# Optimization experiments

Hardware: AMD Instinct MI355X
Metric: run time of the kernel (lower is better)

The kernel has to match this reference:

```python
import jax, jax.numpy as jnp
import numpy as np

ROPE_BASE = 10000.0

def apply_rope(x):
    # x: [B, S, H, Dh]  (rotate-half / NeoX convention)
    B, S, H, Dh = x.shape
    inv_freq = 1.0 / (ROPE_BASE ** (jnp.arange(0, Dh, 2, dtype=jnp.float32) / Dh))  # [Dh/2]
    ang = jnp.arange(S, dtype=jnp.float32)[:, None] * inv_freq[None, :]             # [S, Dh/2]
    cos = jnp.cos(ang)[None, :, None, :].astype(x.dtype)  # [1,S,1,Dh/2]
    sin = jnp.sin(ang)[None, :, None, :].astype(x.dtype)
    x1, x2 = jnp.split(x, 2, axis=-1)
    return jnp.concatenate([x1 * cos - x2 * sin, x1 * sin + x2 * cos], axis=-1)

def setup_inputs() -> dict:
    key = jax.random.key(0)
    k1, k2, k3 = jax.random.split(key, 3)
    B, S, D = 2, 2048, 1024
    x = jax.random.normal(k1, (B, S, D), dtype=jnp.float32)
    attn_mask = jnp.ones((B, S), dtype=bool)
    qkv_w = jax.random.normal(k2, (D, 3 * D), dtype=jnp.float32) * (1.0 / np.sqrt(D))
    out_w = jax.random.normal(k3, (D, D), dtype=jnp.float32) * (1.0 / np.sqrt(D))
    return {"x": x, "qkv_w": qkv_w, "out_w": out_w, "attn_mask": attn_mask, "is_causal": 1}

def reference(x, qkv_w, out_w, attn_mask, is_causal):
    B, S, D = x.shape
    H = 16
    Dh = D // H
    qkv = x @ qkv_w                                  # [B,S,3D]
    q, k, v = jnp.split(qkv, 3, axis=-1)
    q = apply_rope(q.reshape(B, S, H, Dh))           # [B,S,H,Dh]
    k = apply_rope(k.reshape(B, S, H, Dh))
    v = v.reshape(B, S, H, Dh)
    scale = 1.0 / np.sqrt(Dh)
    att = jnp.einsum('bqhd,bkhd->bhqk', q, k) * scale  # [B,H,S,S]
    if is_causal:
        mask = jnp.tril(jnp.ones((S, S), dtype=bool))[None, None]
    else:
        mask = attn_mask[:, None, None, :]             # [B,1,1,S]
    att = jnp.where(mask, att, jnp.finfo(att.dtype).min)
    p = jax.nn.softmax(att, axis=-1)
    y = jnp.einsum('bhqk,bkhd->bqhd', p, v).reshape(B, S, D)
    return y @ out_w
```

## Files before the change

### kernel.cpp

```cpp
#include <hip/hip_runtime.h>
#include <hip/hip_bf16.h>

#define BB 2
#define SS 2048
#define DD 1024
#define HH 16
#define N3 3072

typedef __attribute__((ext_vector_type(8))) short bf16x8;
typedef __attribute__((ext_vector_type(4))) float f32x4;
typedef __attribute__((ext_vector_type(2))) unsigned int u32x2;

__device__ __forceinline__ float b2f(unsigned short u) {
    return __uint_as_float(((unsigned int)u) << 16);
}
__device__ __forceinline__ unsigned short f2b(float f) {
    unsigned int x = __float_as_uint(f);
    x += 0x7fffu + ((x >> 16) & 1u);
    return (unsigned short)(x >> 16);
}
__device__ __forceinline__ unsigned int pack2bf(float a, float b) {
    __hip_bfloat162 h = __float22bfloat162_rn(make_float2(a, b));
    return *(unsigned int*)&h;
}
__device__ __forceinline__ void storeC(float* p, float v) { *p = v; }
__device__ __forceinline__ void storeC(unsigned short* p, float v) { *p = f2b(v); }

__device__ __forceinline__ void gload_lds16(const void* g, void* l) {
    __builtin_amdgcn_global_load_lds(
        (__attribute__((address_space(1))) void*)g,
        (__attribute__((address_space(3))) void*)l, 16, 0, 0);
}

__global__ __launch_bounds__(256) void sincos_tab(float2* __restrict__ tab) {
    int i = blockIdx.x * 256 + threadIdx.x;
    int t = i & 31;
    int s = i >> 5;
    float inv = powf(10000.0f, -(float)t * (1.0f / 32.0f));
    float sn, c;
    sincosf((float)s * inv, &sn, &c);
    tab[i] = make_float2(c, sn);
}

__global__ __launch_bounds__(256) void cast_f32_bf16(
    const float* __restrict__ src, unsigned short* __restrict__ dst)
{
    int i = (blockIdx.x * 256 + threadIdx.x) * 4;
    float4 f = *(const float4*)(src + i);
    uint2 o;
    o.x = pack2bf(f.x, f.y);
    o.y = pack2bf(f.z, f.w);
    *(uint2*)(dst + i) = o;
}

__global__ __launch_bounds__(256) void cast_transpose(
    const float* __restrict__ src, unsigned short* __restrict__ dst,
    int R, int C)
{
    __shared__ unsigned short tile[64][66];
    const int t = threadIdx.x;
    const int c0 = blockIdx.x * 64, r0 = blockIdx.y * 64;
    const int lr = t >> 4;
    const int lc = (t & 15) * 4;
    #pragma unroll
    for (int i = 0; i < 4; ++i) {
        float4 f = *(const float4*)(src + (size_t)(r0 + lr + i * 16) * C + c0 + lc);
        tile[lr + i * 16][lc + 0] = f2b(f.x);
        tile[lr + i * 16][lc + 1] = f2b(f.y);
        tile[lr + i * 16][lc + 2] = f2b(f.z);
        tile[lr + i * 16][lc + 3] = f2b(f.w);
    }
    __syncthreads();
    #pragma unroll
    for (int i = 0; i < 4; ++i) {
        const int wr = lr + i * 16;
        ushort4 o;
        o.x = tile[lc + 0][wr];
        o.y = tile[lc + 1][wr];
        o.z = tile[lc + 2][wr];
        o.w = tile[lc + 3][wr];
        *(ushort4*)(dst + (size_t)(c0 + wr) * R + r0 + lc) = o;
    }
}

template <typename OutT, int TN>
__global__ __launch_bounds__(256) void gemm_mfma(
    const unsigned short* __restrict__ A,
    const unsigned short* __restrict__ Bt,
    OutT* __restrict__ C,
    int M, int N, int K)
{
    constexpr int NI = TN / 32;
    constexpr int NB = TN / 64;
    __shared__ unsigned short Al[128 * 32];
    __shared__ unsigned short Bl[TN * 32];
    const int tid  = threadIdx.x;
    const int wave = tid >> 6;
    const int lane = tid & 63;
    const int quad = lane >> 4;
    const int l16  = lane & 15;
    const int m0 = blockIdx.y * 128;
    const int n0 = blockIdx.x * TN;
    const int wm = (wave >> 1) * 64;
    const int wn = (wave & 1) * (TN / 2);

    const int srowA = wave * 32 + (lane >> 2);
    const int srowB = wave * (16 * NB) + (lane >> 2);
    const int scol  = (lane & 3) * 8;
    const unsigned short* gA = A  + (size_t)(m0 + srowA) * K + scol;
    const unsigned short* gB = Bt + (size_t)(n0 + srowB) * K + scol;

    f32x4 acc[4][NI];
    #pragma unroll
    for (int mi = 0; mi < 4; ++mi)
        #pragma unroll
        for (int ni = 0; ni < NI; ++ni)
            acc[mi][ni] = (f32x4){0.f, 0.f, 0.f, 0.f};

    for (int k0 = 0; k0 < K; k0 += 32) {
        __syncthreads();
        #pragma unroll
        for (int i = 0; i < 2; ++i)
            gload_lds16(gA + (size_t)i * 16 * K + k0, Al + (wave * 2 + i) * 512);
        #pragma unroll
        for (int i = 0; i < NB; ++i)
            gload_lds16(gB + (size_t)i * 16 * K + k0, Bl + (wave * NB + i) * 512);
        __syncthreads();

        bf16x8 af[4], bfr[NI];
        #pragma unroll
        for (int mi = 0; mi < 4; ++mi)
            af[mi] = *(const bf16x8*)&Al[(wm + mi * 16 + l16) * 32 + quad * 8];
        #pragma unroll
        for (int ni = 0; ni < NI; ++ni)
            bfr[ni] = *(const bf16x8*)&Bl[(wn + ni * 16 + l16) * 32 + quad * 8];
        #pragma unroll
        for (int mi = 0; mi < 4; ++mi)
            #pragma unroll
            for (int ni = 0; ni < NI; ++ni)
                acc[mi][ni] = __builtin_amdgcn_mfma_f32_16x16x32_bf16(
                    af[mi], bfr[ni], acc[mi][ni], 0, 0, 0);
    }

    #pragma unroll
    for (int mi = 0; mi < 4; ++mi) {
        #pragma unroll
        for (int r = 0; r < 4; ++r) {
            const size_t base = (size_t)(m0 + wm + mi * 16 + quad * 4 + r) * N + n0 + wn;
            #pragma unroll
            for (int ni = 0; ni < NI; ++ni)
                storeC(&C[base + ni * 16 + l16], acc[mi][ni][r]);
        }
    }
}

__global__ __launch_bounds__(256) void rope_split(
    const unsigned short* __restrict__ qkv,
    const float2* __restrict__ tab,
    unsigned short* __restrict__ qo,
    unsigned short* __restrict__ ko,
    unsigned short* __restrict__ vt)
{
    __shared__ unsigned short Vtile[64][72];

    const float SC = 0.18033688011112042f;
    const int s0 = blockIdx.x * 64;
    const int h  = blockIdx.y;
    const int b  = blockIdx.z;
    const int tid = threadIdx.x;
    const int sl = tid >> 2;
    const int qu = tid & 3;
    const size_t bh = (size_t)b * HH + h;

    const unsigned short* row = qkv + (size_t)(b * SS + s0 + sl) * N3 + h * 64;

    uint4 a0 = *(const uint4*)(row + qu * 8);
    uint4 a1 = *(const uint4*)(row + 32 + qu * 8);
    uint4 b0 = *(const uint4*)(row + DD + qu * 8);
    uint4 b1 = *(const uint4*)(row + DD + 32 + qu * 8);
    uint4 c0 = *(const uint4*)(row + 2 * DD + qu * 8);
    uint4 c1 = *(const uint4*)(row + 2 * DD + 32 + qu * 8);

    float2 cs[8];
    {
        const float4* tp = (const float4*)(tab + (size_t)(s0 + sl) * 32 + qu * 8);
        #pragma unroll
        for (int i = 0; i < 4; ++i) {
            float4 f = tp[i];
            cs[2 * i]     = make_float2(f.x, f.y);
            cs[2 * i + 1] = make_float2(f.z, f.w);
        }
    }

    const unsigned short* pa0 = (const unsigned short*)&a0;
    const unsigned short* pa1 = (const unsigned short*)&a1;
    const unsigned short* pb0 = (const unsigned short*)&b0;
    const unsigned short* pb1 = (const unsigned short*)&b1;
    const unsigned short* pc0 = (const unsigned short*)&c0;
    const unsigned short* pc1 = (const unsigned short*)&c1;

    unsigned short oq1[8], oq2[8], ok1[8], ok2[8];
    #pragma unroll
    for (int j = 0; j < 8; ++j) {
        float c = cs[j].x, sn = cs[j].y;
        float q1 = b2f(pa0[j]), q2 = b2f(pa1[j]);
        float k1 = b2f(pb0[j]), k2 = b2f(pb1[j]);
        oq1[j] = f2b((q1 * c - q2 * sn) * SC);
        oq2[j] = f2b((q1 * sn + q2 * c) * SC);
        ok1[j] = f2b(k1 * c - k2 * sn);
        ok2[j] = f2b(k1 * sn + k2 * c);
        Vtile[qu * 8 + j][sl]      = pc0[j];
        Vtile[32 + qu * 8 + j][sl] = pc1[j];
    }
    const size_t qoff = (bh * SS + s0 + sl) * 64;
    *(uint4*)(qo + qoff + qu * 8)      = *(const uint4*)oq1;
    *(uint4*)(qo + qoff + 32 + qu * 8) = *(const uint4*)oq2;
    *(uint4*)(ko + qoff + qu * 8)      = *(const uint4*)ok1;
    *(uint4*)(ko + qoff + 32 + qu * 8) = *(const uint4*)ok2;

    __syncthreads();

    const int dr = tid >> 2;
    const int ch = tid & 3;
    uint4 t0 = *(const uint4*)&Vtile[dr][ch * 16];
    uint4 t1 = *(const uint4*)&Vtile[dr][ch * 16 + 8];
    unsigned short* vrow = vt + (bh * 64 + dr) * SS + s0 + ch * 16;
    *(uint4*)vrow       = t0;
    *(uint4*)(vrow + 8) = t1;
}

__global__ __launch_bounds__(256) void zero_partials(float* __restrict__ p) {
    int i = (blockIdx.x * 256 + threadIdx.x) * 4;
    *(float4*)(p + i) = make_float4(0.f, 0.f, 0.f, 0.f);
}

__device__ __forceinline__ void attn_step(
    const unsigned short* __restrict__ Kb,
    const unsigned short* __restrict__ Vb,
    const bf16x8 qf0, const bf16x8 qf1, const bf16x8 onesf,
    f32x4 O[4], f32x4& l_acc,
    bool diag, const unsigned char* mrow,
    int kt, int quad, int l16, int csw, int qg)
{
    f32x4 Sf[4];
    #pragma unroll
    for (int st = 0; st < 4; ++st) {
        const unsigned short* kr = &Kb[(st * 16 + l16) * 64];
        bf16x8 kf0 = *(const bf16x8*)(kr + csw * 8);
        bf16x8 kf1 = *(const bf16x8*)(kr + (csw ^ 4) * 8);
        f32x4 s = (f32x4){0.f, 0.f, 0.f, 0.f};
        s = __builtin_amdgcn_mfma_f32_16x16x32_bf16(kf0, qf0, s, 0, 0, 0);
        s = __builtin_amdgcn_mfma_f32_16x16x32_bf16(kf1, qf1, s, 0, 0, 0);
        Sf[st] = s;
    }

    if (diag) {
        #pragma unroll
        for (int st = 0; st < 4; ++st) {
            const int kb0 = kt * 64 + st * 16 + quad * 4;
            #pragma unroll
            for (int r = 0; r < 4; ++r)
                if (kb0 + r > qg) Sf[st][r] = -1e30f;
        }
    } else if (mrow) {
        #pragma unroll
        for (int st = 0; st < 4; ++st) {
            uchar4 mv = *(const uchar4*)(mrow + st * 16 + quad * 4);
            if (!mv.x) Sf[st][0] = -1e30f;
            if (!mv.y) Sf[st][1] = -1e30f;
            if (!mv.z) Sf[st][2] = -1e30f;
            if (!mv.w) Sf[st][3] = -1e30f;
        }
    }

    #pragma unroll
    for (int st = 0; st < 4; ++st)
        #pragma unroll
        for (int r = 0; r < 4; ++r)
            Sf[st][r] = exp2f(Sf[st][r]);

    unsigned int W[4][2];
    #pragma unroll
    for (int st = 0; st < 4; ++st) {
        W[st][0] = pack2bf(Sf[st][0], Sf[st][1]);
        W[st][1] = pack2bf(Sf[st][2], Sf[st][3]);
    }

    unsigned int pw0[4], pw1[4];
    #pragma unroll
    for (int j = 0; j < 2; ++j) {
        u32x2 s1 = __builtin_amdgcn_permlane32_swap(W[0][j], W[1][j], false, false);
        u32x2 s2 = __builtin_amdgcn_permlane16_swap(s1.x, s1.y, false, false);
        pw0[j]     = s2.x;
        pw0[j + 2] = s2.y;
        u32x2 t1 = __builtin_amdgcn_permlane32_swap(W[2][j], W[3][j], false, false);
        u32x2 t2 = __builtin_amdgcn_permlane16_swap(t1.x, t1.y, false, false);
        pw1[j]     = t2.x;
        pw1[j + 2] = t2.y;
    }
    bf16x8 pf0 = *(const bf16x8*)pw0;
    bf16x8 pf1 = *(const bf16x8*)pw1;

    l_acc = __builtin_amdgcn_mfma_f32_16x16x32_bf16(onesf, pf0, l_acc, 0, 0, 0);
    l_acc = __builtin_amdgcn_mfma_f32_16x16x32_bf16(onesf, pf1, l_acc, 0, 0, 0);

    #pragma unroll
    for (int st = 0; st < 4; ++st) {
        const unsigned short* vr = &Vb[(st * 16 + l16) * 64];
        bf16x8 vf0 = *(const bf16x8*)(vr + csw * 8);
        bf16x8 vf1 = *(const bf16x8*)(vr + (csw ^ 4) * 8);
        O[st] = __builtin_amdgcn_mfma_f32_16x16x32_bf16(vf0, pf0, O[st], 0, 0, 0);
        O[st] = __builtin_amdgcn_mfma_f32_16x16x32_bf16(vf1, pf1, O[st], 0, 0, 0);
    }
}

__global__ __launch_bounds__(256) void flash_attn(
    const unsigned short* __restrict__ q,
    const unsigned short* __restrict__ k,
    const unsigned short* __restrict__ vt,
    unsigned short* __restrict__ y,
    float* __restrict__ pO,
    float* __restrict__ pL,
    const int* __restrict__ is_causal,
    const unsigned char* __restrict__ attn_mask)
{
    __shared__ unsigned short Kl[2][64 * 64];
    __shared__ unsigned short Vl[2][64 * 64];

    const int bid  = blockIdx.x;
    const int work = (bid & 7) * 192 + (bid >> 3);
    const int bhi  = work / 48;
    const int s    = work % 48;
    const int b = bhi >> 4;
    const int h = bhi & 15;
    const bool causal = (is_causal[0] != 0);

    int tile, k0t, k1t;
    bool split;
    if (s < 16) {
        tile = 16 + s; k0t = 0; k1t = 15; split = true;
    } else {
        const int r = s - 16, p = r >> 1;
        if (r & 1) { tile = 15 - p; k0t = 0;  k1t = causal ? tile : 31; split = false; }
        else       { tile = 31 - p; k0t = 16; k1t = causal ? tile : 31; split = true;  }
    }

    const int tid  = threadIdx.x;
    const int wave = tid >> 6;
    const int lane = tid & 63;
    const int quad = lane >> 4;
    const int l16  = lane & 15;

    const size_t bh = (size_t)b * HH + h;

    const int qg = tile * 64 + wave * 16 + l16;
    const unsigned short* qrow = q + (bh * SS + qg) * 64;
    const bf16x8 qf0 = *(const bf16x8*)(qrow + quad * 8);
    const bf16x8 qf1 = *(const bf16x8*)(qrow + 32 + quad * 8);

    bf16x8 onesf;
    #pragma unroll
    for (int i = 0; i < 8; ++i) onesf[i] = (short)0x3F80;

    const unsigned short* kbase  = k  + bh * SS * 64;
    const unsigned short* vtbase = vt + bh * 64 * SS;

    const int Rl  = lane >> 3;
    const int cph = lane & 7;
    const int csw = quad ^ (l16 & 7);

    f32x4 O[4];
    #pragma unroll
    for (int st = 0; st < 4; ++st) O[st] = (f32x4){0.f, 0.f, 0.f, 0.f};
    f32x4 l_acc = (f32x4){0.f, 0.f, 0.f, 0.f};

    auto stage = [&](int kt) {
        const int buf = kt & 1;
        #pragma unroll
        for (int i = 0; i < 2; ++i) {
            const int jj = wave * 2 + i;
            const int R  = jj * 8 + Rl;
            const int cl = cph ^ (R & 7);
            gload_lds16(kbase + ((size_t)(kt * 64 + R) * 64 + cl * 8),
                        &Kl[buf][jj * 512]);
            gload_lds16(vtbase + ((size_t)R * SS + kt * 64 + cl * 8),
                        &Vl[buf][jj * 512]);
        }
    };

    stage(k0t);
    for (int kt = k0t; kt <= k1t; ++kt) {
        __syncthreads();
        if (kt + 1 <= k1t) stage(kt + 1);

        const unsigned char* mrow = causal ? nullptr
                                           : (attn_mask + (size_t)b * SS + kt * 64);
        attn_step(Kl[kt & 1], Vl[kt & 1], qf0, qf1, onesf, O, l_acc,
                  causal && kt == tile, mrow, kt, quad, l16, csw, qg);
    }

    if (!split) {
        const float inv = 1.0f / l_acc[0];
        unsigned short* yrow = y + ((size_t)b * SS + qg) * DD + h * 64;
        #pragma unroll
        for (int st = 0; st < 4; ++st) {
            uint2 o;
            o.x = pack2bf(O[st][0] * inv, O[st][1] * inv);
            o.y = pack2bf(O[st][2] * inv, O[st][3] * inv);
            *(uint2*)(yrow + st * 16 + quad * 4) = o;
        }
    } else {
        float* ob = pO + (((bh * 16 + (size_t)(tile - 16)) * 64 + wave * 16 + l16) * 64);
        #pragma unroll
        for (int st = 0; st < 4; ++st)
            #pragma unroll
            for (int r = 0; r < 4; ++r)
                atomicAdd(ob + st * 16 + quad * 4 + r, O[st][r]);
        if (quad == 0)
            atomicAdd(pL + (bh * 16 + (size_t)(tile - 16)) * 64 + wave * 16 + l16,
                      l_acc[0]);
    }
}

__global__ __launch_bounds__(256) void attn_merge(
    const float* __restrict__ pO, const float* __restrict__ pL,
    unsigned short* __restrict__ y)
{
    const int i = (blockIdx.x * 256 + threadIdx.x) * 4;
    float4 o = *(const float4*)(pO + i);
    const int rowi = i >> 6;
    const int d    = i & 63;
    const float inv = 1.0f / pL[rowi];
    const int row = rowi & 63;
    const int tt  = (rowi >> 6) & 15;
    const int bh  = rowi >> 10;
    const int b = bh >> 4, h = bh & 15;
    const int sq = (16 + tt) * 64 + row;
    unsigned short* yp = y + ((size_t)b * SS + sq) * DD + h * 64 + d;
    uint2 ov;
    ov.x = pack2bf(o.x * inv, o.y * inv);
    ov.y = pack2bf(o.z * inv, o.w * inv);
    *(uint2*)yp = ov;
}

extern "C" void kernel_launch(void* const* d_in, const int* in_sizes, int n_in,
                              void* d_out, int out_size, void* d_ws, size_t ws_size,
                              hipStream_t stream) {
    const float* x      = (const float*)d_in[0];
    const float* qkv_w  = (const float*)d_in[1];
    const float* out_w  = (const float*)d_in[2];
    const unsigned char* mask = (const unsigned char*)d_in[3];
    const int*   is_c   = (const int*)d_in[4];
    float* out = (float*)d_out;

    unsigned short* xb  = (unsigned short*)d_ws;
    unsigned short* w1t = xb  + (size_t)4096 * 1024;
    unsigned short* w2t = w1t + (size_t)3072 * 1024;
    unsigned short* qkv = w2t + (size_t)1024 * 1024;
    unsigned short* qb  = qkv + (size_t)4096 * 3072;
    unsigned short* kb  = qb  + (size_t)BB * HH * SS * 64;
    unsigned short* vt  = kb  + (size_t)BB * HH * SS * 64;
    float2* tab = (float2*)(vt + (size_t)BB * HH * SS * 64);
    unsigned short* yb = xb;

    float* pO = (float*)qkv;
    float* pL = pO + (size_t)32 * 16 * 64 * 64;

    sincos_tab<<<(SS * 32) / 256, 256, 0, stream>>>(tab);
    cast_f32_bf16<<<(4096 * 1024) / 1024, 256, 0, stream>>>(x, xb);
    cast_transpose<<<dim3(N3 / 64, DD / 64), 256, 0, stream>>>(qkv_w, w1t, DD, N3);
    cast_transpose<<<dim3(DD / 64, DD / 64), 256, 0, stream>>>(out_w, w2t, DD, DD);

    gemm_mfma<unsigned short, 128><<<dim3(N3 / 128, 4096 / 128), 256, 0, stream>>>(
        xb, w1t, qkv, 4096, N3, DD);

    rope_split<<<dim3(SS / 64, HH, BB), 256, 0, stream>>>(qkv, tab, qb, kb, vt);

    zero_partials<<<2080, 256, 0, stream>>>(pO);

    flash_attn<<<dim3(48 * BB * HH), 256, 0, stream>>>(qb, kb, vt, yb, pO, pL,
                                                       is_c, mask);

    attn_merge<<<2048, 256, 0, stream>>>(pO, pL, yb);

    gemm_mfma<float, 64><<<dim3(DD / 64, 4096 / 128), 256, 0, stream>>>(
        yb, w2t, out, 4096, DD, DD);
}
```

Measured before the change: 233.8 us.

## Replace split-KV atomic accumulation with per-half partial buffers and raise MFMA priority

Each of the two KV halves of a split query tile now writes its partial O and l to its own buffer with plain vector stores, and the merge kernel sums the two halves. This removes the float atomicAdds and the separate zeroing kernel. It doubles the partial buffer footprint and adds one extra read to the merge. It also wraps the MFMA sections of the attention step in s_setprio raises so those waves are favoured while issuing matrix instructions.

```diff
diff --git a/kernel.cpp b/kernel.cpp
--- a/kernel.cpp
+++ b/kernel.cpp
@@ -6,6 +6,9 @@
 #define DD 1024
 #define HH 16
 #define N3 3072
+
+#define POH (32 * 16 * 64 * 64)
+#define PLH (32 * 16 * 64)
 
 typedef __attribute__((ext_vector_type(8))) short bf16x8;
 typedef __attribute__((ext_vector_type(4))) float f32x4;
@@ -229,11 +232,6 @@
     *(uint4*)(vrow + 8) = t1;
 }
 
-__global__ __launch_bounds__(256) void zero_partials(float* __restrict__ p) {
-    int i = (blockIdx.x * 256 + threadIdx.x) * 4;
-    *(float4*)(p + i) = make_float4(0.f, 0.f, 0.f, 0.f);
-}
-
 __device__ __forceinline__ void attn_step(
     const unsigned short* __restrict__ Kb,
     const unsigned short* __restrict__ Vb,
@@ -243,6 +241,7 @@
     int kt, int quad, int l16, int csw, int qg)
 {
     f32x4 Sf[4];
+    __builtin_amdgcn_s_setprio(1);
     #pragma unroll
     for (int st = 0; st < 4; ++st) {
         const unsigned short* kr = &Kb[(st * 16 + l16) * 64];
@@ -253,6 +252,7 @@
         s = __builtin_amdgcn_mfma_f32_16x16x32_bf16(kf1, qf1, s, 0, 0, 0);
         Sf[st] = s;
     }
+    __builtin_amdgcn_s_setprio(0);
 
     if (diag) {
         #pragma unroll
@@ -301,9 +301,9 @@
     bf16x8 pf0 = *(const bf16x8*)pw0;
     bf16x8 pf1 = *(const bf16x8*)pw1;
 
+    __builtin_amdgcn_s_setprio(1);
     l_acc = __builtin_amdgcn_mfma_f32_16x16x32_bf16(onesf, pf0, l_acc, 0, 0, 0);
     l_acc = __builtin_amdgcn_mfma_f32_16x16x32_bf16(onesf, pf1, l_acc, 0, 0, 0);
-
     #pragma unroll
     for (int st = 0; st < 4; ++st) {
         const unsigned short* vr = &Vb[(st * 16 + l16) * 64];
@@ -312,6 +312,7 @@
         O[st] = __builtin_amdgcn_mfma_f32_16x16x32_bf16(vf0, pf0, O[st], 0, 0, 0);
         O[st] = __builtin_amdgcn_mfma_f32_16x16x32_bf16(vf1, pf1, O[st], 0, 0, 0);
     }
+    __builtin_amdgcn_s_setprio(0);
 }
 
 __global__ __launch_bounds__(256) void flash_attn(
@@ -344,6 +345,7 @@
         if (r & 1) { tile = 15 - p; k0t = 0;  k1t = causal ? tile : 31; split = false; }
         else       { tile = 31 - p; k0t = 16; k1t = causal ? tile : 31; split = true;  }
     }
+    const int half = (s < 16) ? 0 : 1;
 
     const int tid  = threadIdx.x;
     const int wave = tid >> 6;
@@ -410,15 +412,14 @@
             *(uint2*)(yrow + st * 16 + quad * 4) = o;
         }
     } else {
-        float* ob = pO + (((bh * 16 + (size_t)(tile - 16)) * 64 + wave * 16 + l16) * 64);
+        float* ob = pO + (size_t)half * POH
+                  + (((bh * 16 + (size_t)(tile - 16)) * 64 + wave * 16 + l16) * 64);
         #pragma unroll
         for (int st = 0; st < 4; ++st)
-            #pragma unroll
-            for (int r = 0; r < 4; ++r)
-                atomicAdd(ob + st * 16 + quad * 4 + r, O[st][r]);
+            *(f32x4*)(ob + st * 16 + quad * 4) = O[st];
         if (quad == 0)
-            atomicAdd(pL + (bh * 16 + (size_t)(tile - 16)) * 64 + wave * 16 + l16,
-                      l_acc[0]);
+            pL[(size_t)half * PLH + (bh * 16 + (size_t)(tile - 16)) * 64
+               + wave * 16 + l16] = l_acc[0];
     }
 }
 
@@ -427,10 +428,11 @@
     unsigned short* __restrict__ y)
 {
     const int i = (blockIdx.x * 256 + threadIdx.x) * 4;
-    float4 o = *(const float4*)(pO + i);
+    float4 oa = *(const float4*)(pO + i);
+    float4 obv = *(const float4*)(pO + POH + i);
     const int rowi = i >> 6;
     const int d    = i & 63;
-    const float inv = 1.0f / pL[rowi];
+    const float inv = 1.0f / (pL[rowi] + pL[PLH + rowi]);
     const int row = rowi & 63;
     const int tt  = (rowi >> 6) & 15;
     const int bh  = rowi >> 10;
@@ -438,8 +440,8 @@
     const int sq = (16 + tt) * 64 + row;
     unsigned short* yp = y + ((size_t)b * SS + sq) * DD + h * 64 + d;
     uint2 ov;
-    ov.x = pack2bf(o.x * inv, o.y * inv);
-    ov.y = pack2bf(o.z * inv, o.w * inv);
+    ov.x = pack2bf((oa.x + obv.x) * inv, (oa.y + obv.y) * inv);
+    ov.y = pack2bf((oa.z + obv.z) * inv, (oa.w + obv.w) * inv);
     *(uint2*)yp = ov;
 }
 
@@ -464,7 +466,7 @@
     unsigned short* yb = xb;
 
     float* pO = (float*)qkv;
-    float* pL = pO + (size_t)32 * 16 * 64 * 64;
+    float* pL = pO + (size_t)2 * POH;
 
     sincos_tab<<<(SS * 32) / 256, 256, 0, stream>>>(tab);
     cast_f32_bf16<<<(4096 * 1024) / 1024, 256, 0, stream>>>(x, xb);
@@ -476,8 +478,6 @@
 
     rope_split<<<dim3(SS / 64, HH, BB), 256, 0, stream>>>(qkv, tab, qb, kb, vt);
 
-    zero_partials<<<2080, 256, 0, stream>>>(pO);
-
     flash_attn<<<dim3(48 * BB * HH), 256, 0, stream>>>(qb, kb, vt, yb, pO, pL,
                                                        is_c, mask);
 
```

Result: faster. 210.6 us (-9.9%).
